# Optimization experiments

Measured on AMD Instinct MI355X. Metric: run time of the kernel, lower is better.

## Reference

```python
import jax, jax.numpy as jnp
import numpy as np

M = 4096      # dictionary_size
D = 64        # feature dim
YD = 4        # output dim (y_dim)
FF = 0.999    # forgetting_factor
REG = 1e-2    # regularisation
JITTER = 1e-10
LS = 8.0      # RBF lengthscale


def rbf(a, b):
    # squared-distance RBF Gram via the ||a||^2 + ||b||^2 - 2ab^T identity
    a2 = jnp.sum(a * a, -1)[:, None]
    b2 = jnp.sum(b * b, -1)[None, :]
    d2 = jnp.maximum(a2 + b2 - 2.0 * (a @ b.T), 0.0)
    return jnp.exp(-d2 / (2.0 * LS * LS))


def setup_inputs() -> dict:
    key = jax.random.key(0)
    ks = jax.random.split(key, 7)
    return {
        'dictionary': jax.random.normal(ks[0], (M, D), jnp.float32),
        'mu': jax.random.normal(ks[1], (YD, M, 1), jnp.float32),
        'sigma': jax.random.normal(ks[2], (M, M), jnp.float32),
        'Q': jax.random.normal(ks[3], (M, M), jnp.float32),
        'x': jax.random.normal(ks[4], (D,), jnp.float32),
        'y': jax.random.normal(ks[5], (YD,), jnp.float32),
        'noise_num': jax.random.uniform(ks[6], (YD, 1, 1), jnp.float32),
        'noise_den': jnp.ones((1,), jnp.float32),
        'time_index': jnp.arange(M, dtype=jnp.float32),
        't': M,
    }


def reference(dictionary, mu, sigma, Q, x, y, noise_num, noise_den, time_index, t):
    alloc = time_index >= 0.0                      # (M,) bool: allocated slots
    y_ = y[:, None, None]                          # (YD,1,1)

    # --- B2P forgetting ---
    Kdd = rbf(dictionary, dictionary) * (alloc[:, None] * alloc[None, :])
    sig = FF * sigma + (1.0 - FF) * Kdd
    mu_f = jnp.sqrt(FF) * mu

    # --- kernel evals for new sample ---
    K_dx = rbf(dictionary, x[None, :]) * alloc[:, None]   # (M,1)
    K_xx = rbf(x[None, :], x[None, :]) + JITTER           # (1,1)

    q_ = Q @ K_dx                                         # (M,1)
    pu = jnp.maximum(K_xx - K_dx.T @ q_, 0.0)             # projection uncertainty (1,1)
    h_ = sig @ q_                                         # (M,1)
    npv = jnp.maximum(pu + q_.T @ h_, 0.0)                # noiseless predictive var (1,1)
    pred_mean = q_.T @ mu_f                               # (YD,1,1) via batched matmul
    pv = REG + npv

    # --- augmented (M+1) state ---
    p_ = jnp.concatenate((h_, npv), axis=-2)              # (M+1,1)
    mu_a = jnp.concatenate((mu_f, pred_mean), axis=-2) + (y_ - pred_mean) / pv * p_
    sig_a = jnp.block([[sig, h_], [h_.T, npv]]) - (p_ @ p_.T) / pv
    p2 = jnp.concatenate((q_, -jnp.ones((1, 1), q_.dtype)), axis=0)
    Q_a = jnp.pad(Q, ((0, 1), (0, 1))) + (p2 @ p2.T) / pu

    nnum = noise_num + FF * (y_ - pred_mean) ** 2 / pv
    nden = noise_den + FF

    # --- pruning criterion ---
    x_alloc = jnp.concatenate((alloc, jnp.ones((1,), bool)))

    def crit_low(_):
        return jnp.concatenate((jnp.ones((M, 1), Q_a.dtype), jnp.zeros((1, 1), Q_a.dtype)))

    def crit_mse(_):
        dq = jnp.where(~x_alloc, jnp.inf, jnp.diag(Q_a))
        errors = Q_a @ mu_a / dq[:, None]                 # (YD,M+1,1)
        return jnp.abs(errors).sum(-3)                    # (M+1,1)

    criterion = jax.lax.cond(pu.squeeze() < JITTER, crit_low, crit_mse, None)
    prune = jnp.argmin(criterion)
    denom = jnp.where(~x_alloc[prune], jnp.inf, Q_a[prune, prune])

    # swap (prune <-> last) permutation, then drop last row/col
    perm = jnp.arange(M + 1)
    perm = jnp.where(perm == prune, M, jnp.where(perm == M, prune, perm))

    Q_r = Q_a[perm, :]                                    # row swap
    Qs = Q_r[:-1, prune]                                  # column `prune` after row swap
    Q_n = Q_r[:, perm][:M, :M] - jnp.outer(Qs, Qs) / denom

    mu_n = mu_a[:, perm, :][:, :M, :]
    sig_n = sig_a[perm, :][:, perm][:M, :M]

    dict_n = dictionary.at[prune].set(x)
    ti_n = time_index.at[prune].set(jnp.asarray(t, time_index.dtype))
    alloc_n = ti_n >= 0.0
    sig_n = (alloc_n[:, None] * alloc_n[None, :]) * sig_n
    mu_n = jnp.where((ti_n < 0.0)[:, None], 0.0, mu_n)

    return (mu_n, sig_n, Q_n, dict_n, ti_n, nnum, nden)
```

## Files before the change

kernel.cpp:

```cpp
#include <hip/hip_runtime.h>
#include <math.h>

#define Mn 4096
#define Dn 64
#define MUA_STRIDE 4104

#define OFF_A2   0
#define OFF_CRIT 0
#define OFF_K    4096
#define OFF_Q    8192
#define OFF_H    12288
#define OFF_MUA  16384
#define OFF_QS   32800
#define OFF_QSD  36896
#define SC_PU    40992
#define SC_INVPU 40993
#define SC_NPV   40994
#define SC_PV    40995
#define SC_INVPV 40996
#define SC_DENOM 40997
#define SC_PRUNE 40998
#define OFF_DICTB 49152

#define O_MU   0
#define O_SIG  16384
#define O_Q    16793600
#define O_DICT 33570816
#define O_TI   33832960
#define O_NNUM 33837056
#define O_NDEN 33837060

typedef __attribute__((ext_vector_type(8))) __bf16 bf16x8;
typedef __attribute__((ext_vector_type(4))) float f32x4;

__device__ __forceinline__ float waveReduceSum(float v) {
#pragma unroll
    for (int o = 32; o > 0; o >>= 1) v += __shfl_down(v, o);
    return v;
}

__device__ __forceinline__ unsigned short f2bf_rne(float f) {
    unsigned u = __float_as_uint(f);
    unsigned r = (u + 0x7FFFu + ((u >> 16) & 1u)) >> 16;
    return (unsigned short)r;
}

__global__ void k1_prep(const float* __restrict__ dict, const float* __restrict__ x,
                        const float* __restrict__ ti, float* __restrict__ ws) {
    int row  = blockIdx.x * 4 + (threadIdx.x >> 6);
    int lane = threadIdx.x & 63;
    float d  = dict[row * Dn + lane];
    float xv = x[lane];
    ((unsigned short*)(ws + OFF_DICTB))[row * Dn + lane] = f2bf_rne(d);
    float a2 = waveReduceSum(d * d);
    float x2 = waveReduceSum(xv * xv);
    float dx = waveReduceSum(d * xv);
    if (lane == 0) {
        ws[OFF_A2 + row] = a2;
        float d2 = fmaxf(a2 + x2 - 2.0f * dx, 0.0f);
        float kv = expf(d2 * (-1.0f / 128.0f));
        ws[OFF_K + row] = (ti[row] >= 0.0f) ? kv : 0.0f;
    }
}

__global__ void k2_q(const float* __restrict__ Q, float* __restrict__ ws) {
    __shared__ float red[4];
    const int row = blockIdx.x;
    const int tid = threadIdx.x;
    const float4* Qr = (const float4*)(Q + (size_t)row * Mn);
    const float4* kv = (const float4*)(ws + OFF_K);
    float s = 0.0f;
#pragma unroll
    for (int it = 0; it < 4; ++it) {
        int u = tid + it * 256;
        float4 a = Qr[u], b = kv[u];
        s += a.x * b.x + a.y * b.y + a.z * b.z + a.w * b.w;
    }
    s = waveReduceSum(s);
    if ((tid & 63) == 0) red[tid >> 6] = s;
    __syncthreads();
    if (tid == 0) {
        ws[OFF_Q + row] = red[0] + red[1] + red[2] + red[3];
        ws[OFF_H + row] = 0.0f;
    }
}

__global__ __launch_bounds__(256) void k3_h(
        const float* __restrict__ sigma, const float* __restrict__ ti,
        float* __restrict__ ws) {
    const int tid  = threadIdx.x;
    const int lane = tid & 63;
    const int w    = tid >> 6;

    if (blockIdx.x < 1024) {
        const int row = blockIdx.x * 4 + w;
        const float4* S  = (const float4*)(sigma + (size_t)row * Mn);
        const float4* q4 = (const float4*)(ws + OFF_Q);
        float s = 0.0f;
#pragma unroll
        for (int it = 0; it < 16; ++it) {
            int u = lane + it * 64;
            float4 a = S[u], b = q4[u];
            s += a.x * b.x + a.y * b.y + a.z * b.z + a.w * b.w;
        }
        s = waveReduceSum(s);
        if (lane == 0) atomicAdd(ws + OFF_H + row, 0.999f * s);
        return;
    }

    const int t  = blockIdx.x - 1024;
    const int i0 = (t >> 5) * 128 + (w >> 1) * 64;
    const int j0 = (t & 31) * 128 + (w & 1) * 64;
    const int lr = lane >> 4;
    const int lc = lane & 15;
    const uint4* db = (const uint4*)(ws + OFF_DICTB);

    bf16x8 bfrag[4][2];
    float a2j[4], qmj[4];
#pragma unroll
    for (int jt = 0; jt < 4; ++jt) {
        const int col = j0 + jt * 16 + lc;
        bfrag[jt][0] = __builtin_bit_cast(bf16x8, db[col * 8 + lr]);
        bfrag[jt][1] = __builtin_bit_cast(bf16x8, db[col * 8 + 4 + lr]);
        a2j[jt] = ws[OFF_A2 + col];
        float alj = (ti[col] >= 0.0f) ? 1.0f : 0.0f;
        qmj[jt] = 0.001f * alj * ws[OFF_Q + col];
    }

#pragma unroll
    for (int it = 0; it < 4; ++it) {
        const int arow = i0 + it * 16 + lc;
        bf16x8 af0 = __builtin_bit_cast(bf16x8, db[arow * 8 + lr]);
        bf16x8 af1 = __builtin_bit_cast(bf16x8, db[arow * 8 + 4 + lr]);
        float hacc[4] = {0.f, 0.f, 0.f, 0.f};
        float a2i[4], ali[4];
#pragma unroll
        for (int i = 0; i < 4; ++i) {
            const int rg = i0 + it * 16 + lr * 4 + i;
            a2i[i] = ws[OFF_A2 + rg];
            ali[i] = (ti[rg] >= 0.0f) ? 1.0f : 0.0f;
        }
#pragma unroll
        for (int jt = 0; jt < 4; ++jt) {
            f32x4 acc = {0.0f, 0.0f, 0.0f, 0.0f};
            acc = __builtin_amdgcn_mfma_f32_16x16x32_bf16(af0, bfrag[jt][0], acc, 0, 0, 0);
            acc = __builtin_amdgcn_mfma_f32_16x16x32_bf16(af1, bfrag[jt][1], acc, 0, 0, 0);
#pragma unroll
            for (int i = 0; i < 4; ++i) {
                float d2 = fmaxf(a2i[i] + a2j[jt] - 2.0f * acc[i], 0.0f);
                float kv = __expf(d2 * (-1.0f / 128.0f)) * ali[i];
                hacc[i] = fmaf(kv, qmj[jt], hacc[i]);
            }
        }
#pragma unroll
        for (int i = 0; i < 4; ++i) {
            float v = hacc[i];
            v += __shfl_xor(v, 1);
            v += __shfl_xor(v, 2);
            v += __shfl_xor(v, 4);
            v += __shfl_xor(v, 8);
            if (lc == i) atomicAdd(ws + OFF_H + i0 + it * 16 + lr * 4 + i, v);
        }
    }
}

__device__ __forceinline__ float blockReduce1024(float v, float* sred) {
    v = waveReduceSum(v);
    int tid = threadIdx.x;
    __syncthreads();
    if ((tid & 63) == 0) sred[tid >> 6] = v;
    __syncthreads();
    float r = 0.0f;
    if (tid == 0) {
#pragma unroll
        for (int i = 0; i < 16; ++i) r += sred[i];
    }
    return r;
}

__global__ __launch_bounds__(1024) void k4_scalars(
        const float* __restrict__ mu, const float* __restrict__ y,
        const float* __restrict__ nn, const float* __restrict__ nd,
        float* __restrict__ ws, float* __restrict__ out) {
    __shared__ float sred[16];
    __shared__ float sb[8];
    const int tid = threadIdx.x;
    const float* k = ws + OFF_K;
    const float* q = ws + OFF_Q;
    const float* h = ws + OFF_H;
    float kq = 0, qh = 0, p0 = 0, p1 = 0, p2 = 0, p3 = 0;
    for (int i = tid; i < Mn; i += 1024) {
        float qi = q[i];
        kq += k[i] * qi;
        qh += qi * h[i];
        p0 += qi * mu[0 * Mn + i];
        p1 += qi * mu[1 * Mn + i];
        p2 += qi * mu[2 * Mn + i];
        p3 += qi * mu[3 * Mn + i];
    }
    float rkq = blockReduce1024(kq, sred);
    float rqh = blockReduce1024(qh, sred);
    float r0 = blockReduce1024(p0, sred);
    float r1 = blockReduce1024(p1, sred);
    float r2 = blockReduce1024(p2, sred);
    float r3 = blockReduce1024(p3, sred);
    if (tid == 0) {
        const float sf = sqrtf(0.999f);
        float pu  = fmaxf(1.0f - rkq, 0.0f);
        float npv = fmaxf(pu + rqh, 0.0f);
        float pv  = 0.01f + npv;
        ws[SC_PU] = pu;
        ws[SC_INVPU] = 1.0f / pu;
        ws[SC_NPV] = npv;
        ws[SC_PV] = pv;
        ws[SC_INVPV] = 1.0f / pv;
        float pm[4] = {sf * r0, sf * r1, sf * r2, sf * r3};
#pragma unroll
        for (int yd = 0; yd < 4; ++yd) {
            float yv = y[yd];
            float dy = yv - pm[yd];
            float dl = dy / pv;
            sb[yd] = dl;
            ws[OFF_MUA + yd * MUA_STRIDE + Mn] = pm[yd] + dl * npv;
            out[O_NNUM + yd] = nn[yd] + 0.999f * (dy * dy) / pv;
        }
        out[O_NDEN] = nd[0] + 0.999f;
    }
    __syncthreads();
    const float sf = sqrtf(0.999f);
    float d0 = sb[0], d1 = sb[1], d2 = sb[2], d3 = sb[3];
    for (int i = tid; i < Mn; i += 1024) {
        float hi = h[i];
        ws[OFF_MUA + 0 * MUA_STRIDE + i] = sf * mu[0 * Mn + i] + d0 * hi;
        ws[OFF_MUA + 1 * MUA_STRIDE + i] = sf * mu[1 * Mn + i] + d1 * hi;
        ws[OFF_MUA + 2 * MUA_STRIDE + i] = sf * mu[2 * Mn + i] + d2 * hi;
        ws[OFF_MUA + 3 * MUA_STRIDE + i] = sf * mu[3 * Mn + i] + d3 * hi;
    }
}

__global__ __launch_bounds__(256) void k5_crit(const float* __restrict__ Q,
                                               const float* __restrict__ ti,
                                               float* __restrict__ ws) {
    __shared__ float sred[4][4];
    const int row = blockIdx.x;
    const int tid = threadIdx.x;
    const float pu = ws[SC_PU];
    if (pu < 1e-10f) {
        if (tid == 0) ws[OFF_CRIT + row] = (row < Mn) ? 1.0f : 0.0f;
        return;
    }
    const float inv_pu = ws[SC_INVPU];
    const bool rin = (row < Mn);
    const float p2i = rin ? ws[OFF_Q + row] : -1.0f;
    const float4* q4  = (const float4*)(ws + OFF_Q);
    const float4* Qr4 = (const float4*)(Q + (size_t)row * Mn);
    const float* mua = ws + OFF_MUA;
    float n0 = 0, n1 = 0, n2 = 0, n3 = 0;
#pragma unroll
    for (int it = 0; it < 4; ++it) {
        int u = tid + it * 256;
        float4 qv = q4[u];
        float4 base = rin ? Qr4[u] : make_float4(0.f, 0.f, 0.f, 0.f);
        float4 qa;
        qa.x = base.x + p2i * qv.x * inv_pu;
        qa.y = base.y + p2i * qv.y * inv_pu;
        qa.z = base.z + p2i * qv.z * inv_pu;
        qa.w = base.w + p2i * qv.w * inv_pu;
        const float4 m0 = *(const float4*)(mua + 0 * MUA_STRIDE + u * 4);
        const float4 m1 = *(const float4*)(mua + 1 * MUA_STRIDE + u * 4);
        const float4 m2 = *(const float4*)(mua + 2 * MUA_STRIDE + u * 4);
        const float4 m3 = *(const float4*)(mua + 3 * MUA_STRIDE + u * 4);
        n0 += qa.x * m0.x + qa.y * m0.y + qa.z * m0.z + qa.w * m0.w;
        n1 += qa.x * m1.x + qa.y * m1.y + qa.z * m1.z + qa.w * m1.w;
        n2 += qa.x * m2.x + qa.y * m2.y + qa.z * m2.z + qa.w * m2.w;
        n3 += qa.x * m3.x + qa.y * m3.y + qa.z * m3.z + qa.w * m3.w;
    }
    n0 = waveReduceSum(n0);
    n1 = waveReduceSum(n1);
    n2 = waveReduceSum(n2);
    n3 = waveReduceSum(n3);
    if ((tid & 63) == 0) {
        int w = tid >> 6;
        sred[w][0] = n0; sred[w][1] = n1; sred[w][2] = n2; sred[w][3] = n3;
    }
    __syncthreads();
    if (tid == 0) {
        float t0 = 0, t1 = 0, t2 = 0, t3 = 0;
#pragma unroll
        for (int w = 0; w < 4; ++w) {
            t0 += sred[w][0]; t1 += sred[w][1]; t2 += sred[w][2]; t3 += sred[w][3];
        }
        float qaM = -p2i * inv_pu;
        t0 += qaM * mua[0 * MUA_STRIDE + Mn];
        t1 += qaM * mua[1 * MUA_STRIDE + Mn];
        t2 += qaM * mua[2 * MUA_STRIDE + Mn];
        t3 += qaM * mua[3 * MUA_STRIDE + Mn];
        bool xa = rin ? (ti[row] >= 0.0f) : true;
        float crit = 0.0f;
        if (xa) {
            float dq = rin ? (Q[(size_t)row * Mn + row] + p2i * p2i * inv_pu) : inv_pu;
            crit = fabsf(t0 / dq) + fabsf(t1 / dq) + fabsf(t2 / dq) + fabsf(t3 / dq);
        }
        ws[OFF_CRIT + row] = crit;
    }
}

__global__ __launch_bounds__(1024) void k6_argmin(const float* __restrict__ Q,
                                                  const float* __restrict__ ti,
                                                  float* __restrict__ ws) {
    __shared__ float sval[1024];
    __shared__ int   sidx[1024];
    const int tid = threadIdx.x;
    float bv = INFINITY;
    int bi = Mn + 1;
    for (int i = tid; i <= Mn; i += 1024) {
        float v = ws[OFF_CRIT + i];
        if (v < bv) { bv = v; bi = i; }
    }
    sval[tid] = bv; sidx[tid] = bi;
    __syncthreads();
    for (int s = 512; s > 0; s >>= 1) {
        if (tid < s) {
            float ov = sval[tid + s]; int oi = sidx[tid + s];
            if (ov < sval[tid] || (ov == sval[tid] && oi < sidx[tid])) {
                sval[tid] = ov; sidx[tid] = oi;
            }
        }
        __syncthreads();
    }
    if (tid == 0) {
        int prune = sidx[0];
        ((int*)ws)[SC_PRUNE] = prune;
        float inv_pu = ws[SC_INVPU];
        bool xa = (prune == Mn) ? true : (ti[prune] >= 0.0f);
        float qap;
        if (prune < Mn) {
            float qp = ws[OFF_Q + prune];
            qap = Q[(size_t)prune * Mn + prune] + qp * qp * inv_pu;
        } else {
            qap = inv_pu;
        }
        ws[SC_DENOM] = xa ? qap : INFINITY;
    }
}

__global__ void k6b_vec(const float* __restrict__ Q, const float* __restrict__ dict,
                        const float* __restrict__ x, const float* __restrict__ ti,
                        const int* __restrict__ tptr, float* __restrict__ ws,
                        float* __restrict__ out) {
    const int tid = blockIdx.x * 256 + threadIdx.x;
    const int prune = ((const int*)ws)[SC_PRUNE];
    const int row = tid >> 6, col = tid & 63;
    out[O_DICT + tid] = (row == prune) ? x[col] : dict[tid];
    if (tid < Mn) {
        float tv = ti[tid];
        if (tid == prune) {
            int raw = *tptr;
            tv = (raw >= 0 && raw < (1 << 30)) ? (float)raw : __int_as_float(raw);
        }
        out[O_TI + tid] = tv;
        const float inv_pu = ws[SC_INVPU];
        const float denom  = ws[SC_DENOM];
        const float p2p = (prune < Mn) ? ws[OFF_Q + prune] : -1.0f;
        float qs;
        if (tid == prune) {
            qs = -p2p * inv_pu;
        } else {
            float base = (prune < Mn) ? Q[(size_t)tid * Mn + prune] : 0.0f;
            qs = base + ws[OFF_Q + tid] * p2p * inv_pu;
        }
        ws[OFF_QS + tid] = qs;
        ws[OFF_QSD + tid] = qs / denom;
    }
}

__global__ __launch_bounds__(256) void k7_fused(const float* __restrict__ Q,
                                                const float* __restrict__ sigma,
                                                const float* __restrict__ ti,
                                                float* __restrict__ out,
                                                const float* __restrict__ ws) {
    const int tid = threadIdx.x;
    const int prune = ((const int*)ws)[SC_PRUNE];
    const float inv_pu = ws[SC_INVPU];
    const float inv_pv = ws[SC_INVPV];
    const float npv = ws[SC_NPV];

    if (blockIdx.x < 4096) {
        const int i = blockIdx.x;
        const int pi = (i == prune) ? Mn : i;
        const bool piok = (pi < Mn);
        const float p2i = piok ? ws[OFF_Q + pi] : -1.0f;
        const float qsi = ws[OFF_QS + i];
        const float4* Qr4  = (const float4*)(Q + (size_t)pi * Mn);
        const float4* q4   = (const float4*)(ws + OFF_Q);
        const float4* qsd4 = (const float4*)(ws + OFF_QSD);
        float4* o4 = (float4*)(out + O_Q + (size_t)i * Mn);
#pragma unroll
        for (int it = 0; it < 4; ++it) {
            int u = tid + it * 256;
            float4 base = piok ? Qr4[u] : make_float4(0.f, 0.f, 0.f, 0.f);
            float4 p2j = q4[u];
            if ((prune >> 2) == u) {
                int c = prune & 3;
                ((float*)&p2j)[c] = -1.0f;
                ((float*)&base)[c] = 0.0f;
            }
            float4 d = qsd4[u];
            float4 r;
            r.x = base.x + p2i * p2j.x * inv_pu - qsi * d.x;
            r.y = base.y + p2i * p2j.y * inv_pu - qsi * d.y;
            r.z = base.z + p2i * p2j.z * inv_pu - qsi * d.z;
            r.w = base.w + p2i * p2j.w * inv_pu - qsi * d.w;
            o4[u] = r;
        }
        if (tid < 4) {
            float tin = out[O_TI + i];
            float v;
            if (tin < 0.0f) v = 0.0f;
            else v = ws[OFF_MUA + tid * MUA_STRIDE + ((i == prune) ? Mn : i)];
            out[O_MU + tid * Mn + i] = v;
        }
        return;
    }

    const int t    = blockIdx.x - 4096;
    const int lane = tid & 63;
    const int w    = tid >> 6;
    const int i0 = (t >> 5) * 128 + (w >> 1) * 64;
    const int j0 = (t & 31) * 128 + (w & 1) * 64;
    const int lr = lane >> 4;
    const int lc = lane & 15;
    const uint4* db = (const uint4*)(ws + OFF_DICTB);

    bf16x8 bfrag[4][2];
    float a2j[4], hj[4], aljo[4], ajn[4];
    bool pcol[4];
#pragma unroll
    for (int jt = 0; jt < 4; ++jt) {
        const int col = j0 + jt * 16 + lc;
        bfrag[jt][0] = __builtin_bit_cast(bf16x8, db[col * 8 + lr]);
        bfrag[jt][1] = __builtin_bit_cast(bf16x8, db[col * 8 + 4 + lr]);
        a2j[jt]  = ws[OFF_A2 + col];
        hj[jt]   = ws[OFF_H + col];
        aljo[jt] = (ti[col] >= 0.0f) ? 1.0f : 0.0f;
        ajn[jt]  = (out[O_TI + col] >= 0.0f) ? 1.0f : 0.0f;
        pcol[jt] = (col == prune);
    }

#pragma unroll
    for (int it = 0; it < 4; ++it) {
        const int arow = i0 + it * 16 + lc;
        bf16x8 af0 = __builtin_bit_cast(bf16x8, db[arow * 8 + lr]);
        bf16x8 af1 = __builtin_bit_cast(bf16x8, db[arow * 8 + 4 + lr]);
        float a2i[4], alio[4], ain[4], hr[4];
        bool prow[4];
#pragma unroll
        for (int i = 0; i < 4; ++i) {
            const int rg = i0 + it * 16 + lr * 4 + i;
            a2i[i]  = ws[OFF_A2 + rg];
            alio[i] = (ti[rg] >= 0.0f) ? 1.0f : 0.0f;
            ain[i]  = (out[O_TI + rg] >= 0.0f) ? 1.0f : 0.0f;
            hr[i]   = ws[OFF_H + rg];
            prow[i] = (rg == prune);
        }
#pragma unroll
        for (int jt = 0; jt < 4; ++jt) {
            f32x4 acc = {0.0f, 0.0f, 0.0f, 0.0f};
            acc = __builtin_amdgcn_mfma_f32_16x16x32_bf16(af0, bfrag[jt][0], acc, 0, 0, 0);
            acc = __builtin_amdgcn_mfma_f32_16x16x32_bf16(af1, bfrag[jt][1], acc, 0, 0, 0);
            const int colg = j0 + jt * 16 + lc;
#pragma unroll
            for (int i = 0; i < 4; ++i) {
                const int rg = i0 + it * 16 + lr * 4 + i;
                const size_t off = (size_t)rg * Mn + colg;
                float sv = sigma[off];
                float d2 = fmaxf(a2i[i] + a2j[jt] - 2.0f * acc[i], 0.0f);
                float kv = __expf(d2 * (-1.0f / 128.0f)) * alio[i] * aljo[jt];
                float bs = 0.999f * sv + 0.001f * kv;
                if (pcol[jt]) bs = prow[i] ? npv : hr[i];
                if (prow[i])  bs = pcol[jt] ? npv : hj[jt];
                float p_i = prow[i]  ? npv : hr[i];
                float p_j = pcol[jt] ? npv : hj[jt];
                float r = ain[i] * ajn[jt] * (bs - p_i * p_j * inv_pv);
                out[O_SIG + off] = r;
            }
        }
    }
}

extern "C" void kernel_launch(void* const* d_in, const int* in_sizes, int n_in,
                              void* d_out, int out_size, void* d_ws, size_t ws_size,
                              hipStream_t stream) {
    const float* dict  = (const float*)d_in[0];
    const float* mu    = (const float*)d_in[1];
    const float* sigma = (const float*)d_in[2];
    const float* Q     = (const float*)d_in[3];
    const float* x     = (const float*)d_in[4];
    const float* y     = (const float*)d_in[5];
    const float* nn    = (const float*)d_in[6];
    const float* nd    = (const float*)d_in[7];
    const float* ti    = (const float*)d_in[8];
    const int*   tptr  = (const int*)d_in[9];
    float* out = (float*)d_out;
    float* ws  = (float*)d_ws;

    k1_prep<<<1024, 256, 0, stream>>>(dict, x, ti, ws);
    k2_q<<<4096, 256, 0, stream>>>(Q, ws);
    k3_h<<<2048, 256, 0, stream>>>(sigma, ti, ws);
    k4_scalars<<<1, 1024, 0, stream>>>(mu, y, nn, nd, ws, out);
    k5_crit<<<4097, 256, 0, stream>>>(Q, ti, ws);
    k6_argmin<<<1, 1024, 0, stream>>>(Q, ti, ws);
    k6b_vec<<<1024, 256, 0, stream>>>(Q, dict, x, ti, tptr, ws, out);
    k7_fused<<<5120, 256, 0, stream>>>(Q, sigma, ti, out, ws);
}
```

Before: 369.3 us.

## Derive prune criterion algebraically, drop mu_a buffer, vectorize sigma tile stores

The criterion kernel now computes Q·mu, Q·h per row (one wave per row) and reconstructs Q_a·mu_a with scalar corrections from k4, avoiding materialising the augmented mu in workspace and the extra q-vector load. The augmented-row criterion is computed once in k4. In the fused sigma kernel, MFMA operands are swapped so each lane owns four contiguous columns, enabling float4 sigma loads and output stores, and the row-tile blocks are scheduled first. This trades extra FMA work and changed rounding order for reduced memory traffic and better coalescing.

```diff
diff --git a/kernel.cpp b/kernel.cpp
--- a/kernel.cpp
+++ b/kernel.cpp
@@ -3,14 +3,12 @@
 
 #define Mn 4096
 #define Dn 64
-#define MUA_STRIDE 4104
 
 #define OFF_A2   0
-#define OFF_CRIT 0
 #define OFF_K    4096
 #define OFF_Q    8192
 #define OFF_H    12288
-#define OFF_MUA  16384
+#define OFF_CRIT 20480
 #define OFF_QS   32800
 #define OFF_QSD  36896
 #define SC_PU    40992
@@ -20,6 +18,9 @@
 #define SC_INVPV 40996
 #define SC_DENOM 40997
 #define SC_PRUNE 40998
+#define SC_DL    41000
+#define SC_VY    41004
+#define SC_MUAM  41008
 #define OFF_DICTB 49152
 
 #define O_MU   0
@@ -183,7 +184,6 @@
         const float* __restrict__ nn, const float* __restrict__ nd,
         float* __restrict__ ws, float* __restrict__ out) {
     __shared__ float sred[16];
-    __shared__ float sb[8];
     const int tid = threadIdx.x;
     const float* k = ws + OFF_K;
     const float* q = ws + OFF_Q;
@@ -214,94 +214,74 @@
         ws[SC_NPV] = npv;
         ws[SC_PV] = pv;
         ws[SC_INVPV] = 1.0f / pv;
-        float pm[4] = {sf * r0, sf * r1, sf * r2, sf * r3};
+        float rr[4] = {r0, r1, r2, r3};
+        float critM = 0.0f;
 #pragma unroll
         for (int yd = 0; yd < 4; ++yd) {
-            float yv = y[yd];
-            float dy = yv - pm[yd];
+            float pm = sf * rr[yd];
+            float dy = y[yd] - pm;
             float dl = dy / pv;
-            sb[yd] = dl;
-            ws[OFF_MUA + yd * MUA_STRIDE + Mn] = pm[yd] + dl * npv;
+            float muaM = pm + dl * npv;
+            float vy   = (sf * rr[yd] + dl * rqh) - muaM;
+            ws[SC_DL + yd]   = dl;
+            ws[SC_VY + yd]   = vy;
+            ws[SC_MUAM + yd] = muaM;
+            critM += fabsf(vy);
             out[O_NNUM + yd] = nn[yd] + 0.999f * (dy * dy) / pv;
         }
         out[O_NDEN] = nd[0] + 0.999f;
-    }
-    __syncthreads();
-    const float sf = sqrtf(0.999f);
-    float d0 = sb[0], d1 = sb[1], d2 = sb[2], d3 = sb[3];
-    for (int i = tid; i < Mn; i += 1024) {
-        float hi = h[i];
-        ws[OFF_MUA + 0 * MUA_STRIDE + i] = sf * mu[0 * Mn + i] + d0 * hi;
-        ws[OFF_MUA + 1 * MUA_STRIDE + i] = sf * mu[1 * Mn + i] + d1 * hi;
-        ws[OFF_MUA + 2 * MUA_STRIDE + i] = sf * mu[2 * Mn + i] + d2 * hi;
-        ws[OFF_MUA + 3 * MUA_STRIDE + i] = sf * mu[3 * Mn + i] + d3 * hi;
+        ws[OFF_CRIT + Mn] = (pu < 1e-10f) ? 0.0f : critM;
     }
 }
 
 __global__ __launch_bounds__(256) void k5_crit(const float* __restrict__ Q,
+                                               const float* __restrict__ mu,
                                                const float* __restrict__ ti,
                                                float* __restrict__ ws) {
-    __shared__ float sred[4][4];
-    const int row = blockIdx.x;
-    const int tid = threadIdx.x;
+    const int row  = blockIdx.x * 4 + (threadIdx.x >> 6);
+    const int lane = threadIdx.x & 63;
     const float pu = ws[SC_PU];
     if (pu < 1e-10f) {
-        if (tid == 0) ws[OFF_CRIT + row] = (row < Mn) ? 1.0f : 0.0f;
+        if (lane == 0) ws[OFF_CRIT + row] = 1.0f;
         return;
     }
-    const float inv_pu = ws[SC_INVPU];
-    const bool rin = (row < Mn);
-    const float p2i = rin ? ws[OFF_Q + row] : -1.0f;
-    const float4* q4  = (const float4*)(ws + OFF_Q);
     const float4* Qr4 = (const float4*)(Q + (size_t)row * Mn);
-    const float* mua = ws + OFF_MUA;
-    float n0 = 0, n1 = 0, n2 = 0, n3 = 0;
-#pragma unroll
-    for (int it = 0; it < 4; ++it) {
-        int u = tid + it * 256;
-        float4 qv = q4[u];
-        float4 base = rin ? Qr4[u] : make_float4(0.f, 0.f, 0.f, 0.f);
-        float4 qa;
-        qa.x = base.x + p2i * qv.x * inv_pu;
-        qa.y = base.y + p2i * qv.y * inv_pu;
-        qa.z = base.z + p2i * qv.z * inv_pu;
-        qa.w = base.w + p2i * qv.w * inv_pu;
-        const float4 m0 = *(const float4*)(mua + 0 * MUA_STRIDE + u * 4);
-        const float4 m1 = *(const float4*)(mua + 1 * MUA_STRIDE + u * 4);
-        const float4 m2 = *(const float4*)(mua + 2 * MUA_STRIDE + u * 4);
-        const float4 m3 = *(const float4*)(mua + 3 * MUA_STRIDE + u * 4);
-        n0 += qa.x * m0.x + qa.y * m0.y + qa.z * m0.z + qa.w * m0.w;
-        n1 += qa.x * m1.x + qa.y * m1.y + qa.z * m1.z + qa.w * m1.w;
-        n2 += qa.x * m2.x + qa.y * m2.y + qa.z * m2.z + qa.w * m2.w;
-        n3 += qa.x * m3.x + qa.y * m3.y + qa.z * m3.z + qa.w * m3.w;
-    }
-    n0 = waveReduceSum(n0);
-    n1 = waveReduceSum(n1);
-    n2 = waveReduceSum(n2);
-    n3 = waveReduceSum(n3);
-    if ((tid & 63) == 0) {
-        int w = tid >> 6;
-        sred[w][0] = n0; sred[w][1] = n1; sred[w][2] = n2; sred[w][3] = n3;
-    }
-    __syncthreads();
-    if (tid == 0) {
-        float t0 = 0, t1 = 0, t2 = 0, t3 = 0;
-#pragma unroll
-        for (int w = 0; w < 4; ++w) {
-            t0 += sred[w][0]; t1 += sred[w][1]; t2 += sred[w][2]; t3 += sred[w][3];
-        }
-        float qaM = -p2i * inv_pu;
-        t0 += qaM * mua[0 * MUA_STRIDE + Mn];
-        t1 += qaM * mua[1 * MUA_STRIDE + Mn];
-        t2 += qaM * mua[2 * MUA_STRIDE + Mn];
-        t3 += qaM * mua[3 * MUA_STRIDE + Mn];
-        bool xa = rin ? (ti[row] >= 0.0f) : true;
+    const float4* m04 = (const float4*)(mu + 0 * Mn);
+    const float4* m14 = (const float4*)(mu + 1 * Mn);
+    const float4* m24 = (const float4*)(mu + 2 * Mn);
+    const float4* m34 = (const float4*)(mu + 3 * Mn);
+    const float4* h4  = (const float4*)(ws + OFF_H);
+    float am0 = 0, am1 = 0, am2 = 0, am3 = 0, ah = 0;
+#pragma unroll
+    for (int it = 0; it < 16; ++it) {
+        int u = lane + it * 64;
+        float4 qv = Qr4[u];
+        float4 a0 = m04[u], a1 = m14[u], a2 = m24[u], a3 = m34[u], hh = h4[u];
+        am0 += qv.x * a0.x + qv.y * a0.y + qv.z * a0.z + qv.w * a0.w;
+        am1 += qv.x * a1.x + qv.y * a1.y + qv.z * a1.z + qv.w * a1.w;
+        am2 += qv.x * a2.x + qv.y * a2.y + qv.z * a2.z + qv.w * a2.w;
+        am3 += qv.x * a3.x + qv.y * a3.y + qv.z * a3.z + qv.w * a3.w;
+        ah  += qv.x * hh.x + qv.y * hh.y + qv.z * hh.z + qv.w * hh.w;
+    }
+    am0 = waveReduceSum(am0);
+    am1 = waveReduceSum(am1);
+    am2 = waveReduceSum(am2);
+    am3 = waveReduceSum(am3);
+    ah  = waveReduceSum(ah);
+    if (lane == 0) {
+        const float inv_pu = ws[SC_INVPU];
+        const float sf = sqrtf(0.999f);
+        float qrow = ws[OFF_Q + row];
+        float dq = Q[(size_t)row * Mn + row] + qrow * qrow * inv_pu;
         float crit = 0.0f;
-        if (xa) {
-            float dq = rin ? (Q[(size_t)row * Mn + row] + p2i * p2i * inv_pu) : inv_pu;
-            crit = fabsf(t0 / dq) + fabsf(t1 / dq) + fabsf(t2 / dq) + fabsf(t3 / dq);
-        }
-        ws[OFF_CRIT + row] = crit;
+        float am[4] = {am0, am1, am2, am3};
+#pragma unroll
+        for (int yd = 0; yd < 4; ++yd) {
+            float e = sf * am[yd] + ws[SC_DL + yd] * ah + ws[SC_VY + yd] * inv_pu * qrow;
+            crit += fabsf(e / dq);
+        }
+        bool xa = (ti[row] >= 0.0f);
+        ws[OFF_CRIT + row] = xa ? crit : 0.0f;
     }
 }
 
@@ -376,6 +356,7 @@
 
 __global__ __launch_bounds__(256) void k7_fused(const float* __restrict__ Q,
                                                 const float* __restrict__ sigma,
+                                                const float* __restrict__ mu,
                                                 const float* __restrict__ ti,
                                                 float* __restrict__ out,
                                                 const float* __restrict__ ws) {
@@ -385,8 +366,8 @@
     const float inv_pv = ws[SC_INVPV];
     const float npv = ws[SC_NPV];
 
-    if (blockIdx.x < 4096) {
-        const int i = blockIdx.x;
+    if (blockIdx.x >= 1024) {
+        const int i = blockIdx.x - 1024;
         const int pi = (i == prune) ? Mn : i;
         const bool piok = (pi < Mn);
         const float p2i = piok ? ws[OFF_Q + pi] : -1.0f;
@@ -417,13 +398,17 @@
             float tin = out[O_TI + i];
             float v;
             if (tin < 0.0f) v = 0.0f;
-            else v = ws[OFF_MUA + tid * MUA_STRIDE + ((i == prune) ? Mn : i)];
+            else if (i == prune) v = ws[SC_MUAM + tid];
+            else {
+                const float sf = sqrtf(0.999f);
+                v = sf * mu[tid * Mn + i] + ws[SC_DL + tid] * ws[OFF_H + i];
+            }
             out[O_MU + tid * Mn + i] = v;
         }
         return;
     }
 
-    const int t    = blockIdx.x - 4096;
+    const int t    = blockIdx.x;
     const int lane = tid & 63;
     const int w    = tid >> 6;
     const int i0 = (t >> 5) * 128 + (w >> 1) * 64;
@@ -432,58 +417,61 @@
     const int lc = lane & 15;
     const uint4* db = (const uint4*)(ws + OFF_DICTB);
 
-    bf16x8 bfrag[4][2];
-    float a2j[4], hj[4], aljo[4], ajn[4];
-    bool pcol[4];
+    bf16x8 bfI[4][2];
+    float a2i_s[4], alio_s[4], ain_s[4], hr_s[4];
+    bool prow_s[4];
+#pragma unroll
+    for (int it = 0; it < 4; ++it) {
+        const int ri = i0 + it * 16 + lc;
+        bfI[it][0] = __builtin_bit_cast(bf16x8, db[ri * 8 + lr]);
+        bfI[it][1] = __builtin_bit_cast(bf16x8, db[ri * 8 + 4 + lr]);
+        a2i_s[it]  = ws[OFF_A2 + ri];
+        alio_s[it] = (ti[ri] >= 0.0f) ? 1.0f : 0.0f;
+        ain_s[it]  = (out[O_TI + ri] >= 0.0f) ? 1.0f : 0.0f;
+        hr_s[it]   = ws[OFF_H + ri];
+        prow_s[it] = (ri == prune);
+    }
+
 #pragma unroll
     for (int jt = 0; jt < 4; ++jt) {
-        const int col = j0 + jt * 16 + lc;
-        bfrag[jt][0] = __builtin_bit_cast(bf16x8, db[col * 8 + lr]);
-        bfrag[jt][1] = __builtin_bit_cast(bf16x8, db[col * 8 + 4 + lr]);
-        a2j[jt]  = ws[OFF_A2 + col];
-        hj[jt]   = ws[OFF_H + col];
-        aljo[jt] = (ti[col] >= 0.0f) ? 1.0f : 0.0f;
-        ajn[jt]  = (out[O_TI + col] >= 0.0f) ? 1.0f : 0.0f;
-        pcol[jt] = (col == prune);
-    }
-
-#pragma unroll
-    for (int it = 0; it < 4; ++it) {
-        const int arow = i0 + it * 16 + lc;
-        bf16x8 af0 = __builtin_bit_cast(bf16x8, db[arow * 8 + lr]);
-        bf16x8 af1 = __builtin_bit_cast(bf16x8, db[arow * 8 + 4 + lr]);
-        float a2i[4], alio[4], ain[4], hr[4];
-        bool prow[4];
-#pragma unroll
-        for (int i = 0; i < 4; ++i) {
-            const int rg = i0 + it * 16 + lr * 4 + i;
-            a2i[i]  = ws[OFF_A2 + rg];
-            alio[i] = (ti[rg] >= 0.0f) ? 1.0f : 0.0f;
-            ain[i]  = (out[O_TI + rg] >= 0.0f) ? 1.0f : 0.0f;
-            hr[i]   = ws[OFF_H + rg];
-            prow[i] = (rg == prune);
-        }
-#pragma unroll
-        for (int jt = 0; jt < 4; ++jt) {
+        const int jrow = j0 + jt * 16 + lc;
+        bf16x8 afJ0 = __builtin_bit_cast(bf16x8, db[jrow * 8 + lr]);
+        bf16x8 afJ1 = __builtin_bit_cast(bf16x8, db[jrow * 8 + 4 + lr]);
+        const int cb = j0 + jt * 16 + lr * 4;
+        const float4 a2j4 = *(const float4*)(ws + OFF_A2 + cb);
+        const float4 hj4  = *(const float4*)(ws + OFF_H + cb);
+        const float4 tio4 = *(const float4*)(ti + cb);
+        const float4 tin4 = *(const float4*)(out + O_TI + cb);
+        float a2j[4] = {a2j4.x, a2j4.y, a2j4.z, a2j4.w};
+        float hj[4]  = {hj4.x, hj4.y, hj4.z, hj4.w};
+        float aljo[4] = {tio4.x >= 0.f ? 1.f : 0.f, tio4.y >= 0.f ? 1.f : 0.f,
+                         tio4.z >= 0.f ? 1.f : 0.f, tio4.w >= 0.f ? 1.f : 0.f};
+        float ajn[4]  = {tin4.x >= 0.f ? 1.f : 0.f, tin4.y >= 0.f ? 1.f : 0.f,
+                         tin4.z >= 0.f ? 1.f : 0.f, tin4.w >= 0.f ? 1.f : 0.f};
+        bool pcol[4] = {cb + 0 == prune, cb + 1 == prune, cb + 2 == prune, cb + 3 == prune};
+#pragma unroll
+        for (int it = 0; it < 4; ++it) {
             f32x4 acc = {0.0f, 0.0f, 0.0f, 0.0f};
-            acc = __builtin_amdgcn_mfma_f32_16x16x32_bf16(af0, bfrag[jt][0], acc, 0, 0, 0);
-            acc = __builtin_amdgcn_mfma_f32_16x16x32_bf16(af1, bfrag[jt][1], acc, 0, 0, 0);
-            const int colg = j0 + jt * 16 + lc;
-#pragma unroll
-            for (int i = 0; i < 4; ++i) {
-                const int rg = i0 + it * 16 + lr * 4 + i;
-                const size_t off = (size_t)rg * Mn + colg;
-                float sv = sigma[off];
-                float d2 = fmaxf(a2i[i] + a2j[jt] - 2.0f * acc[i], 0.0f);
-                float kv = __expf(d2 * (-1.0f / 128.0f)) * alio[i] * aljo[jt];
-                float bs = 0.999f * sv + 0.001f * kv;
-                if (pcol[jt]) bs = prow[i] ? npv : hr[i];
-                if (prow[i])  bs = pcol[jt] ? npv : hj[jt];
-                float p_i = prow[i]  ? npv : hr[i];
-                float p_j = pcol[jt] ? npv : hj[jt];
-                float r = ain[i] * ajn[jt] * (bs - p_i * p_j * inv_pv);
-                out[O_SIG + off] = r;
+            acc = __builtin_amdgcn_mfma_f32_16x16x32_bf16(afJ0, bfI[it][0], acc, 0, 0, 0);
+            acc = __builtin_amdgcn_mfma_f32_16x16x32_bf16(afJ1, bfI[it][1], acc, 0, 0, 0);
+            const int rg = i0 + it * 16 + lc;
+            const size_t off = (size_t)rg * Mn + cb;
+            const float4 sv4 = *(const float4*)(sigma + off);
+            float sv[4] = {sv4.x, sv4.y, sv4.z, sv4.w};
+            float res[4];
+#pragma unroll
+            for (int e = 0; e < 4; ++e) {
+                float d2 = fmaxf(a2i_s[it] + a2j[e] - 2.0f * acc[e], 0.0f);
+                float kv = __expf(d2 * (-1.0f / 128.0f)) * alio_s[it] * aljo[e];
+                float bs = 0.999f * sv[e] + 0.001f * kv;
+                if (pcol[e])    bs = prow_s[it] ? npv : hr_s[it];
+                if (prow_s[it]) bs = pcol[e] ? npv : hj[e];
+                float p_i = prow_s[it] ? npv : hr_s[it];
+                float p_j = pcol[e] ? npv : hj[e];
+                res[e] = ain_s[it] * ajn[e] * (bs - p_i * p_j * inv_pv);
             }
+            float4 r4 = {res[0], res[1], res[2], res[3]};
+            *(float4*)(out + O_SIG + off) = r4;
         }
     }
 }
@@ -508,8 +496,8 @@
     k2_q<<<4096, 256, 0, stream>>>(Q, ws);
     k3_h<<<2048, 256, 0, stream>>>(sigma, ti, ws);
     k4_scalars<<<1, 1024, 0, stream>>>(mu, y, nn, nd, ws, out);
-    k5_crit<<<4097, 256, 0, stream>>>(Q, ti, ws);
+    k5_crit<<<1024, 256, 0, stream>>>(Q, mu, ti, ws);
     k6_argmin<<<1, 1024, 0, stream>>>(Q, ti, ws);
     k6b_vec<<<1024, 256, 0, stream>>>(Q, dict, x, ti, tptr, ws, out);
-    k7_fused<<<5120, 256, 0, stream>>>(Q, sigma, ti, out, ws);
-}
+    k7_fused<<<5120, 256, 0, stream>>>(Q, sigma, mu, ti, out, ws);
+}
```

Measured after the change: 337.1 us. 1.1x faster.
